# Optimization experiments

Hardware: AMD Instinct MI355X
Metric: run time of the kernel (lower is better)

The kernel has to match this reference:

```python
import jax, jax.numpy as jnp
import numpy as np

IN_CH = 32
HID = 2 * IN_CH          # 64
MASK_CH = 8 * 27         # 216


def conv3d(x, w, b, replicate_pad):
    # x: [B,C,D,H,W], w: [O,I,kd,kh,kw]
    if replicate_pad:
        x = jnp.pad(x, ((0, 0), (0, 0), (1, 1), (1, 1), (1, 1)), mode='edge')
    y = jax.lax.conv_general_dilated(
        x, w, window_strides=(1, 1, 1), padding='VALID',
        dimension_numbers=('NCDHW', 'OIDHW', 'NCDHW'))
    return y + b[None, :, None, None, None]


def unfold27(x):
    # replicate-padded 3x3x3 neighborhoods -> [B,C,D,H,W,27], n = kd*9+kh*3+kw
    B, C, D, H, W = x.shape
    xp = jnp.pad(x, ((0, 0), (0, 0), (1, 1), (1, 1), (1, 1)), mode='edge')
    patches = [xp[:, :, dz:dz + D, dy:dy + H, dx:dx + W]
               for dz in range(3) for dy in range(3) for dx in range(3)]
    return jnp.stack(patches, axis=-1)


def setup_inputs() -> dict:
    key = jax.random.key(0)
    ks = jax.random.split(key, 6)
    B, C, D, H, W = 1, IN_CH, 48, 48, 48
    x = jax.random.normal(ks[0], (B, C, D, H, W), dtype=jnp.float32)
    features = jax.random.normal(ks[1], (B, IN_CH, D, H, W), dtype=jnp.float32)
    # Conv(in, 2*in, k=3, replicate pad) ; Conv(2*in, 8*27, k=1, zeros pad)
    w1 = jax.random.normal(ks[2], (HID, IN_CH, 3, 3, 3), dtype=jnp.float32) * (1.0 / np.sqrt(IN_CH * 27))
    b1 = jnp.zeros((HID,), dtype=jnp.float32)
    w2 = jax.random.normal(ks[3], (MASK_CH, HID, 1, 1, 1), dtype=jnp.float32) * (1.0 / np.sqrt(HID))
    b2 = jnp.zeros((MASK_CH,), dtype=jnp.float32)
    return {"x": x, "features": features, "w1": w1, "b1": b1, "w2": w2, "b2": b2}


def reference(x, features, w1, b1, w2, b2):
    B, C, D, H, W = x.shape
    # mask network: Conv3 (replicate) -> SiLU -> Conv1 (zeros)
    h = jax.nn.silu(conv3d(features, w1, b1, replicate_pad=True))
    m = conv3d(h, w2, b2, replicate_pad=False)          # [B,216,D,H,W]
    # view(B,1,2,2,2,27,D,H,W).permute(0,1,6,2,7,3,8,4,5) -> [B,D,2,H,2,W,2,27]
    m = m.reshape(B, 2, 2, 2, 27, D, H, W)
    m = jnp.transpose(m, (0, 5, 1, 6, 2, 7, 3, 4))      # b d i h j w k n
    m = jax.nn.softmax(m, axis=-1)
    xu = unfold27(x)                                    # [B,C,D,H,W,27]
    # convex combination: contract over the 27 taps (batched small matmul)
    out = jnp.einsum('bdihjwkn,bcdhwn->bcdihjwk', m, xu)
    return out.reshape(B, C, 2 * D, 2 * H, 2 * W)
```

## Files before the change

### kernel.cpp

```cpp
#include <hip/hip_runtime.h>
#include <math.h>

#define NVOX 110592

typedef _Float16 f16x8 __attribute__((ext_vector_type(8)));
typedef _Float16 f16x4 __attribute__((ext_vector_type(4)));
typedef _Float16 f16x2 __attribute__((ext_vector_type(2)));
typedef float    f32x4 __attribute__((ext_vector_type(4)));

__device__ __forceinline__ float comp4(const float4& v, int j) {
    return j == 0 ? v.x : (j == 1 ? v.y : (j == 2 ? v.z : v.w));
}

__device__ __forceinline__ int xcd_swizzle(int bx, int nwg) {
    int chunk = nwg >> 3;
    return (bx & 7) * chunk + (bx >> 3);
}

__global__ __launch_bounds__(256) void k_prep(
    const float* __restrict__ feat, const float* __restrict__ x,
    const float* __restrict__ w1, const float* __restrict__ w2,
    _Float16* __restrict__ featT, float* __restrict__ xT32,
    _Float16* __restrict__ w1h, _Float16* __restrict__ w2h)
{
    __shared__ float tileb[64 * 34];
    int bx = blockIdx.x;
    int t = threadIdx.x;

    if (bx >= 3456) {
        int e = (bx - 3456) * 256 + t;
        if (e < 64 * 32 * 27) {
            int oc = e / 864;
            int r = e - oc * 864;
            int ci = r / 27;
            int tap = r - ci * 27;
            w1h[oc * 864 + tap * 32 + ci] = (_Float16)w1[e];
        }
        int e2 = e - 55296;
        if (e2 >= 0 && e2 < 224 * 64) {
            int oc = e2 >> 6, k = e2 & 63;
            w2h[e2] = (oc < 216) ? (_Float16)w2[oc * 64 + k] : (_Float16)0.f;
        }
        return;
    }

    if (bx < 1728) {
        _Float16* tile = (_Float16*)tileb;
        int v0 = bx * 64;
        for (int i = t; i < 1024; i += 256) {
            int c2 = i >> 6, dv = i & 63;
            f16x2 v;
            v.x = (_Float16)feat[(2 * c2) * NVOX + v0 + dv];
            v.y = (_Float16)feat[(2 * c2 + 1) * NVOX + v0 + dv];
            *(f16x2*)(tile + dv * 36 + c2 * 2) = v;
        }
        __syncthreads();
        for (int i = t; i < 512; i += 256) {
            int dv = i >> 3, ch = i & 7;
            f16x4 v = *(const f16x4*)(tile + dv * 36 + ch * 4);
            *(f16x4*)(featT + (v0 + dv) * 32 + ch * 4) = v;
        }
        return;
    }

    {
        int v0 = (bx - 1728) * 64;
        for (int i = t; i < 1024; i += 256) {
            int c2 = i >> 6, dv = i & 63;
            float2 v;
            v.x = x[(2 * c2) * NVOX + v0 + dv];
            v.y = x[(2 * c2 + 1) * NVOX + v0 + dv];
            *(float2*)(tileb + dv * 34 + c2 * 2) = v;
        }
        __syncthreads();
        for (int i = t; i < 1024; i += 256) {
            int dv = i >> 4, ch = i & 15;
            float2 v = *(const float2*)(tileb + dv * 34 + ch * 2);
            *(float2*)(xT32 + (size_t)(v0 + dv) * 32 + ch * 2) = v;
        }
    }
}

__global__ __launch_bounds__(512, 4) void k_main(
    const _Float16* __restrict__ featT, const float* __restrict__ xT32,
    const _Float16* __restrict__ w1h, const float* __restrict__ b1,
    const _Float16* __restrict__ w2h, const float* __restrict__ b2,
    float* __restrict__ out)
{
    __shared__ float smem[19752];
    float* mbuf = smem;
    _Float16* X  = (_Float16*)(smem + 10752);
    _Float16* hl = (_Float16*)(smem + 10752);

    int bx = xcd_swizzle(blockIdx.x, gridDim.x);
    int d = bx / 48, hh = bx - d * 48;
    int t = threadIdx.x;

    for (int i = t; i < 1800; i += 512) {
        int col = i >> 2, chunk = i & 3;
        int dzdy = col / 50;
        int px = col - dzdy * 50;
        int dz = dzdy / 3, dy = dzdy - dz * 3;
        int zz = min(max(d + dz - 1, 0), 47);
        int yy = min(max(hh + dy - 1, 0), 47);
        int xx = min(max(px - 1, 0), 47);
        int vox = (zz * 48 + yy) * 48 + xx;
        *(f16x8*)(X + col * 40 + chunk * 8) =
            *(const f16x8*)(featT + vox * 32 + chunk * 8);
    }
    __syncthreads();

    int wid = t >> 6;
    int lane = t & 63;
    int mcol = lane & 15;
    int q = lane >> 4;

    f32x4 c1a = {0.f, 0.f, 0.f, 0.f};
    f32x4 c1b = {0.f, 0.f, 0.f, 0.f};
    int pxb = wid >> 1;
    int och = wid & 1;
    if (wid < 6) {
        const _Float16* wb0 = w1h + (och * 32 + mcol) * 864 + q * 8;
        const _Float16* wb1 = wb0 + 16 * 864;
#pragma unroll 3
        for (int dzdy = 0; dzdy < 9; ++dzdy) {
            const _Float16* brow = X + (dzdy * 50 + pxb * 16 + mcol) * 40 + q * 8;
            const _Float16* wr0 = wb0 + dzdy * 96;
            const _Float16* wr1 = wb1 + dzdy * 96;
#pragma unroll
            for (int dx = 0; dx < 3; ++dx) {
                f16x8 bv = *(const f16x8*)(brow + dx * 40);
                f16x8 a0 = *(const f16x8*)(wr0 + dx * 32);
                f16x8 a1 = *(const f16x8*)(wr1 + dx * 32);
                c1a = __builtin_amdgcn_mfma_f32_16x16x32_f16(a0, bv, c1a, 0, 0, 0);
                c1b = __builtin_amdgcn_mfma_f32_16x16x32_f16(a1, bv, c1b, 0, 0, 0);
            }
        }
    }
    __syncthreads();

    if (wid < 6) {
        int pxv = pxb * 16 + mcol;
        float4 bva = ((const float4*)b1)[(och * 2) * 4 + q];
        float4 bvb = ((const float4*)b1)[(och * 2 + 1) * 4 + q];
        f16x4 o; float s;
        s = c1a[0] + bva.x; o.x = (_Float16)(s / (1.f + __expf(-s)));
        s = c1a[1] + bva.y; o.y = (_Float16)(s / (1.f + __expf(-s)));
        s = c1a[2] + bva.z; o.z = (_Float16)(s / (1.f + __expf(-s)));
        s = c1a[3] + bva.w; o.w = (_Float16)(s / (1.f + __expf(-s)));
        *(f16x4*)(hl + pxv * 72 + och * 32 + q * 4) = o;
        s = c1b[0] + bvb.x; o.x = (_Float16)(s / (1.f + __expf(-s)));
        s = c1b[1] + bvb.y; o.y = (_Float16)(s / (1.f + __expf(-s)));
        s = c1b[2] + bvb.z; o.z = (_Float16)(s / (1.f + __expf(-s)));
        s = c1b[3] + bvb.w; o.w = (_Float16)(s / (1.f + __expf(-s)));
        *(f16x4*)(hl + pxv * 72 + och * 32 + 16 + q * 4) = o;
    }
    __syncthreads();

    for (int tt = wid; tt < 42; tt += 8) {
        int mt = tt / 3, nt = tt - mt * 3;
        float bias[4];
#pragma unroll
        for (int rr = 0; rr < 4; ++rr) {
            int oc = mt * 16 + q * 4 + rr;
            bias[rr] = (oc < 216) ? b2[oc] : 0.f;
        }
        f32x4 acc = {bias[0], bias[1], bias[2], bias[3]};
#pragma unroll
        for (int ks = 0; ks < 2; ++ks) {
            f16x8 av = *(const f16x8*)(w2h + (mt * 16 + mcol) * 64 + ks * 32 + q * 8);
            f16x8 bv = *(const f16x8*)(hl + (nt * 16 + mcol) * 72 + ks * 32 + q * 8);
            acc = __builtin_amdgcn_mfma_f32_16x16x32_f16(av, bv, acc, 0, 0, 0);
        }
        int vox = nt * 16 + mcol;
#pragma unroll
        for (int rr = 0; rr < 4; ++rr) {
            int oc = mt * 16 + q * 4 + rr;
            if (oc < 216) {
                int sub = oc / 27;
                int n = oc - sub * 27;
                mbuf[(sub * 48 + vox) * 28 + n] = acc[rr];
            }
        }
    }
    __syncthreads();

    if (t < 384) {
        int sub = t / 48;
        int vox = t - sub * 48;
        float4* p4p = (float4*)(mbuf + (sub * 48 + vox) * 28);
        float4 v[7];
#pragma unroll
        for (int g = 0; g < 7; ++g) v[g] = p4p[g];
        float mx = fmaxf(fmaxf(v[6].x, v[6].y), v[6].z);
#pragma unroll
        for (int g = 0; g < 6; ++g)
            mx = fmaxf(mx, fmaxf(fmaxf(v[g].x, v[g].y), fmaxf(v[g].z, v[g].w)));
        float s = 0.f;
#pragma unroll
        for (int g = 0; g < 7; ++g) {
            v[g].x = __expf(v[g].x - mx);
            v[g].y = __expf(v[g].y - mx);
            v[g].z = __expf(v[g].z - mx);
            v[g].w = __expf(v[g].w - mx);
        }
        v[6].w = 0.f;
#pragma unroll
        for (int g = 0; g < 7; ++g) s += v[g].x + v[g].y + v[g].z + v[g].w;
        float inv = 1.f / s;
#pragma unroll
        for (int g = 0; g < 7; ++g) {
            v[g].x *= inv; v[g].y *= inv; v[g].z *= inv; v[g].w *= inv;
            p4p[g] = v[g];
        }
    }
    __syncthreads();

    if (t < 384) {
        int cq = t & 7;
        int tx = (t >> 3) & 7;
        int half = (t >> 6) & 1;
        int wig = t >> 7;
        int w = half * 24 + wig * 8 + tx;

        int rb[9];
#pragma unroll
        for (int r = 0; r < 9; ++r) {
            int dz = r / 3, dy = r - (r / 3) * 3;
            int zz = min(max(d + dz - 1, 0), 47);
            int yy = min(max(hh + dy - 1, 0), 47);
            rb[r] = (zz * 48 + yy) * 48;
        }
        int xs0 = max(w - 1, 0), xs2 = min(w + 1, 47);

        float acc[8][4];
#pragma unroll
        for (int sub = 0; sub < 8; ++sub)
#pragma unroll
            for (int cc = 0; cc < 4; ++cc) acc[sub][cc] = 0.f;

        const float4* smem4 = (const float4*)smem;
#pragma unroll
        for (int g = 0; g < 7; ++g) {
            float4 p[8];
#pragma unroll
            for (int sub = 0; sub < 8; ++sub)
                p[sub] = smem4[(sub * 48 + w) * 7 + g];
#pragma unroll
            for (int j = 0; j < 4; ++j) {
                int n = g * 4 + j;
                if (n < 27) {
                    int r = n / 3;
                    int dx = n - r * 3;
                    int xx = (dx == 0) ? xs0 : ((dx == 1) ? w : xs2);
                    float4 xv = *(const float4*)(xT32 +
                                  (size_t)(rb[r] + xx) * 32 + cq * 4);
#pragma unroll
                    for (int sub = 0; sub < 8; ++sub) {
                        float pv = comp4(p[sub], j);
                        acc[sub][0] = fmaf(xv.x, pv, acc[sub][0]);
                        acc[sub][1] = fmaf(xv.y, pv, acc[sub][1]);
                        acc[sub][2] = fmaf(xv.z, pv, acc[sub][2]);
                        acc[sub][3] = fmaf(xv.w, pv, acc[sub][3]);
                    }
                }
            }
        }

#pragma unroll
        for (int ij = 0; ij < 4; ++ij) {
            int i_ = ij >> 1, j_ = ij & 1;
            int rowz = 2 * d + i_;
            int rowy = 2 * hh + j_;
            int s0 = ij * 2;
#pragma unroll
            for (int cc = 0; cc < 4; ++cc) {
                int c = cq * 4 + cc;
                float2 v;
                v.x = acc[s0][cc];
                v.y = acc[s0 + 1][cc];
                *(float2*)(out + (((size_t)c * 96 + rowz) * 96 + rowy) * 96 + 2 * w) = v;
            }
        }
    }
}

extern "C" void kernel_launch(void* const* d_in, const int* in_sizes, int n_in,
                              void* d_out, int out_size, void* d_ws, size_t ws_size,
                              hipStream_t stream) {
    const float* x    = (const float*)d_in[0];
    const float* feat = (const float*)d_in[1];
    const float* w1   = (const float*)d_in[2];
    const float* b1   = (const float*)d_in[3];
    const float* w2   = (const float*)d_in[4];
    const float* b2   = (const float*)d_in[5];
    float* out = (float*)d_out;

    _Float16* w1h   = (_Float16*)d_ws;
    _Float16* w2h   = (_Float16*)((char*)d_ws + 110592);
    _Float16* featT = (_Float16*)((char*)d_ws + 139264);
    float*    xT32  = (float*)((char*)d_ws + 7217152);

    k_prep<<<3728, 256, 0, stream>>>(feat, x, w1, w2, featT, xT32, w1h, w2h);
    k_main<<<2304, 512, 0, stream>>>(featT, xT32, w1h, b1, w2h, b2, out);
}
```

Before: 278.0 us.

## Store x in fp16 and stage its 3x3 neighborhood in shared memory

The transposed copy of x is now stored in half precision, which halves its write and read traffic. The main kernel loads the 9-row neighborhood halo of x into shared memory, reusing the region freed after the conv stage. The convex-combination loop then reads taps from LDS instead of gathering them from global memory, and the thread-to-channel mapping is swapped. This lowers precision on the x values used in the final combination, which may affect accuracy tolerance.

```diff
diff --git a/kernel.cpp b/kernel.cpp
--- a/kernel.cpp
+++ b/kernel.cpp
@@ -20,10 +20,10 @@
 __global__ __launch_bounds__(256) void k_prep(
     const float* __restrict__ feat, const float* __restrict__ x,
     const float* __restrict__ w1, const float* __restrict__ w2,
-    _Float16* __restrict__ featT, float* __restrict__ xT32,
+    _Float16* __restrict__ featT, _Float16* __restrict__ xT,
     _Float16* __restrict__ w1h, _Float16* __restrict__ w2h)
 {
-    __shared__ float tileb[64 * 34];
+    __shared__ _Float16 tile[64 * 36];
     int bx = blockIdx.x;
     int t = threadIdx.x;
 
@@ -44,45 +44,28 @@
         return;
     }
 
-    if (bx < 1728) {
-        _Float16* tile = (_Float16*)tileb;
-        int v0 = bx * 64;
-        for (int i = t; i < 1024; i += 256) {
-            int c2 = i >> 6, dv = i & 63;
-            f16x2 v;
-            v.x = (_Float16)feat[(2 * c2) * NVOX + v0 + dv];
-            v.y = (_Float16)feat[(2 * c2 + 1) * NVOX + v0 + dv];
-            *(f16x2*)(tile + dv * 36 + c2 * 2) = v;
-        }
-        __syncthreads();
-        for (int i = t; i < 512; i += 256) {
-            int dv = i >> 3, ch = i & 7;
-            f16x4 v = *(const f16x4*)(tile + dv * 36 + ch * 4);
-            *(f16x4*)(featT + (v0 + dv) * 32 + ch * 4) = v;
-        }
-        return;
-    }
-
-    {
-        int v0 = (bx - 1728) * 64;
-        for (int i = t; i < 1024; i += 256) {
-            int c2 = i >> 6, dv = i & 63;
-            float2 v;
-            v.x = x[(2 * c2) * NVOX + v0 + dv];
-            v.y = x[(2 * c2 + 1) * NVOX + v0 + dv];
-            *(float2*)(tileb + dv * 34 + c2 * 2) = v;
-        }
-        __syncthreads();
-        for (int i = t; i < 1024; i += 256) {
-            int dv = i >> 4, ch = i & 15;
-            float2 v = *(const float2*)(tileb + dv * 34 + ch * 2);
-            *(float2*)(xT32 + (size_t)(v0 + dv) * 32 + ch * 2) = v;
-        }
+    int which = bx >= 1728;
+    int v0 = (which ? bx - 1728 : bx) * 64;
+    const float* s = which ? x : feat;
+    _Float16* dt = which ? xT : featT;
+
+    for (int i = t; i < 1024; i += 256) {
+        int c2 = i >> 6, dv = i & 63;
+        f16x2 v;
+        v.x = (_Float16)s[(2 * c2) * NVOX + v0 + dv];
+        v.y = (_Float16)s[(2 * c2 + 1) * NVOX + v0 + dv];
+        *(f16x2*)(tile + dv * 36 + c2 * 2) = v;
+    }
+    __syncthreads();
+    for (int i = t; i < 512; i += 256) {
+        int dv = i >> 3, ch = i & 7;
+        f16x4 v = *(const f16x4*)(tile + dv * 36 + ch * 4);
+        *(f16x4*)(dt + (v0 + dv) * 32 + ch * 4) = v;
     }
 }
 
 __global__ __launch_bounds__(512, 4) void k_main(
-    const _Float16* __restrict__ featT, const float* __restrict__ xT32,
+    const _Float16* __restrict__ featT, const _Float16* __restrict__ xT,
     const _Float16* __restrict__ w1h, const float* __restrict__ b1,
     const _Float16* __restrict__ w2h, const float* __restrict__ b2,
     float* __restrict__ out)
@@ -185,6 +168,18 @@
     }
     __syncthreads();
 
+    for (int i = t; i < 1800; i += 512) {
+        int col = i >> 2, chunk = i & 3;
+        int dzdy = col / 50;
+        int px = col - dzdy * 50;
+        int dz = dzdy / 3, dy = dzdy - dz * 3;
+        int zz = min(max(d + dz - 1, 0), 47);
+        int yy = min(max(hh + dy - 1, 0), 47);
+        int xx = min(max(px - 1, 0), 47);
+        int vox = (zz * 48 + yy) * 48 + xx;
+        *(f16x8*)(X + col * 40 + chunk * 8) =
+            *(const f16x8*)(xT + vox * 32 + chunk * 8);
+    }
     if (t < 384) {
         int sub = t / 48;
         int vox = t - sub * 48;
@@ -217,21 +212,11 @@
     __syncthreads();
 
     if (t < 384) {
-        int cq = t & 7;
-        int tx = (t >> 3) & 7;
+        int tx = t & 7;
+        int cq = (t >> 3) & 7;
         int half = (t >> 6) & 1;
         int wig = t >> 7;
         int w = half * 24 + wig * 8 + tx;
-
-        int rb[9];
-#pragma unroll
-        for (int r = 0; r < 9; ++r) {
-            int dz = r / 3, dy = r - (r / 3) * 3;
-            int zz = min(max(d + dz - 1, 0), 47);
-            int yy = min(max(hh + dy - 1, 0), 47);
-            rb[r] = (zz * 48 + yy) * 48;
-        }
-        int xs0 = max(w - 1, 0), xs2 = min(w + 1, 47);
 
         float acc[8][4];
 #pragma unroll
@@ -252,9 +237,10 @@
                 if (n < 27) {
                     int r = n / 3;
                     int dx = n - r * 3;
-                    int xx = (dx == 0) ? xs0 : ((dx == 1) ? w : xs2);
-                    float4 xv = *(const float4*)(xT32 +
-                                  (size_t)(rb[r] + xx) * 32 + cq * 4);
+                    int col = r * 50 + w + dx;
+                    f16x4 xr = *(const f16x4*)(X + col * 40 + cq * 4);
+                    float4 xv = make_float4((float)xr.x, (float)xr.y,
+                                            (float)xr.z, (float)xr.w);
 #pragma unroll
                     for (int sub = 0; sub < 8; ++sub) {
                         float pv = comp4(p[sub], j);
@@ -299,8 +285,8 @@
     _Float16* w1h   = (_Float16*)d_ws;
     _Float16* w2h   = (_Float16*)((char*)d_ws + 110592);
     _Float16* featT = (_Float16*)((char*)d_ws + 139264);
-    float*    xT32  = (float*)((char*)d_ws + 7217152);
-
-    k_prep<<<3728, 256, 0, stream>>>(feat, x, w1, w2, featT, xT32, w1h, w2h);
-    k_main<<<2304, 512, 0, stream>>>(featT, xT32, w1h, b1, w2h, b2, out);
-}
+    _Float16* xT    = (_Float16*)((char*)d_ws + 7217152);
+
+    k_prep<<<3728, 256, 0, stream>>>(feat, x, w1, w2, featT, xT, w1h, w2h);
+    k_main<<<2304, 512, 0, stream>>>(featT, xT, w1h, b1, w2h, b2, out);
+}
```

Measured after the change: 308.9 us. +11.1%, slower.
